# Kernel tuning notes

Measured on AMD Instinct MI355X. Metric: run time of the kernel, lower is better.

## Reference

```python
import jax, jax.numpy as jnp
import numpy as np

N_NODES = 25000
N_EDGES = 400000
D = 1024


def setup_inputs() -> dict:
    key = jax.random.key(0)
    ks = jax.random.split(key, 8)
    s = 1.0 / np.sqrt(D)
    return {
        "x": jax.random.normal(ks[0], (N_NODES, D), dtype=jnp.float32),
        "edge_src": jax.random.randint(ks[1], (N_EDGES,), 0, N_NODES, dtype=jnp.int32),
        "edge_dst": jax.random.randint(ks[2], (N_EDGES,), 0, N_NODES, dtype=jnp.int32),
        "W_self0": jax.random.normal(ks[3], (D, D), dtype=jnp.float32) * s,
        "W_neigh0": jax.random.normal(ks[4], (D, D), dtype=jnp.float32) * s,
        "b0": jnp.zeros((D,), dtype=jnp.float32),
        "W_self1": jax.random.normal(ks[5], (D, D), dtype=jnp.float32) * s,
        "W_neigh1": jax.random.normal(ks[6], (D, D), dtype=jnp.float32) * s,
        "b1": jnp.zeros((D,), dtype=jnp.float32),
    }


def _sage_layer(h, edge_src, edge_dst, deg_inv, W_self, W_neigh, b):
    # mean aggregation over in-neighbors: gather src feats, segment-sum by dst
    msg = h[edge_src]                                            # [E, d]
    agg = jax.ops.segment_sum(msg, edge_dst, num_segments=h.shape[0])  # [N, d]
    mean = agg * deg_inv[:, None]
    return h @ W_self + mean @ W_neigh + b


def reference(x, edge_src, edge_dst, W_self0, W_neigh0, b0, W_self1, W_neigh1, b1):
    N = x.shape[0]
    deg = jax.ops.segment_sum(jnp.ones_like(edge_dst, dtype=x.dtype), edge_dst, num_segments=N)
    deg_inv = 1.0 / jnp.maximum(deg, 1.0)  # isolated nodes -> 0 neighbor mean
    h = jax.nn.relu(_sage_layer(x, edge_src, edge_dst, deg_inv, W_self0, W_neigh0, b0))
    out = _sage_layer(h, edge_src, edge_dst, deg_inv, W_self1, W_neigh1, b1)
    return out
```

## Files before the change

kernel.cpp:

```cpp
#include <hip/hip_runtime.h>
#include <stdint.h>

#define NN 25000
#define NE 400000
#define DD 1024

typedef __attribute__((ext_vector_type(8))) short short8;
typedef __attribute__((ext_vector_type(4))) float f32x4;

__device__ __forceinline__ unsigned short f2bf(float f) {
  union { float f; uint32_t u; } v; v.f = f;
  uint32_t r = v.u + 0x7fffu + ((v.u >> 16) & 1u);
  return (unsigned short)(r >> 16);
}
__device__ __forceinline__ float bf2f(unsigned short h) {
  union { uint32_t u; float f; } v; v.u = ((uint32_t)h) << 16;
  return v.f;
}

__device__ __forceinline__ void gld_lds16(const void* g, void* l) {
  __builtin_amdgcn_global_load_lds(
      (const __attribute__((address_space(1))) void*)g,
      (__attribute__((address_space(3))) void*)l, 16, 0, 0);
}

__global__ __launch_bounds__(256) void k_cast_bf16(const float* __restrict__ in,
                                                   unsigned short* __restrict__ out,
                                                   int n8) {
  int i = blockIdx.x * blockDim.x + threadIdx.x;
  int stride = gridDim.x * blockDim.x;
  for (; i < n8; i += stride) {
    const float4* p = (const float4*)(in + (size_t)i * 8);
    float4 a = p[0], b = p[1];
    ushort4 r0, r1;
    r0.x = f2bf(a.x); r0.y = f2bf(a.y); r0.z = f2bf(a.z); r0.w = f2bf(a.w);
    r1.x = f2bf(b.x); r1.y = f2bf(b.y); r1.z = f2bf(b.z); r1.w = f2bf(b.w);
    ushort4* q = (ushort4*)(out + (size_t)i * 8);
    q[0] = r0; q[1] = r1;
  }
}

__global__ __launch_bounds__(256) void k_transcast(const float* __restrict__ W,
                                                   unsigned short* __restrict__ WT,
                                                   int kofs) {
  __shared__ unsigned short tile[64][66];
  int t = threadIdx.x;
  int k0 = blockIdx.x * 64, n0 = blockIdx.y * 64;
#pragma unroll
  for (int p = 0; p < 16; ++p) {
    int idx = p * 256 + t;
    int lr = idx >> 6, lc = idx & 63;
    tile[lr][lc] = f2bf(W[(size_t)(k0 + lr) * 1024 + n0 + lc]);
  }
  __syncthreads();
#pragma unroll
  for (int p = 0; p < 16; ++p) {
    int idx = p * 256 + t;
    int lr = idx >> 6, lc = idx & 63;
    WT[(size_t)(n0 + lr) * 2048 + kofs + k0 + lc] = tile[lc][lr];
  }
}

__global__ __launch_bounds__(256) void k_deg(const int* __restrict__ dst,
                                             int* __restrict__ deg, int E) {
  int i = blockIdx.x * blockDim.x + threadIdx.x;
  if (i < E) atomicAdd(&deg[dst[i]], 1);
}

__global__ __launch_bounds__(1024) void k_scan(const int* __restrict__ deg,
                                               int* __restrict__ rowptr,
                                               int* __restrict__ cursor,
                                               float* __restrict__ deg_inv, int N) {
  __shared__ int wsum[16];
  __shared__ int carry_s;
  int t = threadIdx.x, lane = t & 63, w = t >> 6;
  if (t == 0) carry_s = 0;
  __syncthreads();
  for (int base = 0; base < N; base += 1024) {
    int i = base + t;
    int v = (i < N) ? deg[i] : 0;
    int x = v;
#pragma unroll
    for (int off = 1; off < 64; off <<= 1) {
      int y = __shfl_up(x, off);
      if (lane >= off) x += y;
    }
    __syncthreads();
    if (lane == 63) wsum[w] = x;
    __syncthreads();
    if (w == 0 && lane < 16) {
      int s = wsum[lane];
#pragma unroll
      for (int off = 1; off < 16; off <<= 1) {
        int y = __shfl_up(s, off);
        if (lane >= off) s += y;
      }
      wsum[lane] = s;
    }
    __syncthreads();
    int wbase = (w > 0) ? wsum[w - 1] : 0;
    int incl = wbase + x;
    int carry = carry_s;
    if (i < N) {
      int excl = carry + incl - v;
      rowptr[i] = excl;
      cursor[i] = excl;
      deg_inv[i] = 1.0f / fmaxf((float)v, 1.0f);
    }
    __syncthreads();
    if (t == 1023) carry_s = carry + incl;
  }
  __syncthreads();
  if (t == 0) rowptr[N] = carry_s;
}

__global__ __launch_bounds__(256) void k_fill(const int* __restrict__ src,
                                              const int* __restrict__ dst,
                                              int* __restrict__ cursor,
                                              int* __restrict__ srcs, int E) {
  int i = blockIdx.x * blockDim.x + threadIdx.x;
  if (i < E) {
    int p = atomicAdd(&cursor[dst[i]], 1);
    srcs[p] = src[i];
  }
}

__global__ __launch_bounds__(256) void k_agg(const unsigned short* __restrict__ h,
                                             const int* __restrict__ rowptr,
                                             const int* __restrict__ srcs,
                                             const float* __restrict__ deg_inv,
                                             unsigned short* __restrict__ mean) {
  int node = blockIdx.x;
  int t = threadIdx.x;
  int beg = rowptr[node], end = rowptr[node + 1];
  int c = t * 4;
  float a0 = 0.f, a1 = 0.f, a2 = 0.f, a3 = 0.f;
  int e = beg;
  for (; e + 1 < end; e += 2) {
    int s0 = srcs[e], s1 = srcs[e + 1];
    ushort4 v0 = *(const ushort4*)(h + (size_t)s0 * DD + c);
    ushort4 v1 = *(const ushort4*)(h + (size_t)s1 * DD + c);
    a0 += bf2f(v0.x) + bf2f(v1.x);
    a1 += bf2f(v0.y) + bf2f(v1.y);
    a2 += bf2f(v0.z) + bf2f(v1.z);
    a3 += bf2f(v0.w) + bf2f(v1.w);
  }
  if (e < end) {
    int s0 = srcs[e];
    ushort4 v0 = *(const ushort4*)(h + (size_t)s0 * DD + c);
    a0 += bf2f(v0.x); a1 += bf2f(v0.y); a2 += bf2f(v0.z); a3 += bf2f(v0.w);
  }
  float di = deg_inv[node];
  ushort4 r;
  r.x = f2bf(a0 * di); r.y = f2bf(a1 * di); r.z = f2bf(a2 * di); r.w = f2bf(a3 * di);
  *(ushort4*)(mean + (size_t)node * DD + c) = r;
}

template <bool RELU, bool OUT_BF16>
__global__ __launch_bounds__(256) void k_gemm(const unsigned short* __restrict__ A1,
                                              const unsigned short* __restrict__ A2,
                                              const unsigned short* __restrict__ WT,
                                              const float* __restrict__ bias,
                                              void* __restrict__ Cout, int M) {
  __shared__ __align__(16) unsigned short lA[128 * 32];
  __shared__ __align__(16) unsigned short lB[128 * 32];
  const int t = threadIdx.x;
  const int lane = t & 63, wave = t >> 6;
  const int wm = wave >> 1, wn = wave & 1;
  const int bn = blockIdx.x, bm = blockIdx.y;
  const int fr = lane & 15, fq = lane >> 4;

  f32x4 acc[4][4];
#pragma unroll
  for (int m = 0; m < 4; ++m)
#pragma unroll
    for (int n = 0; n < 4; ++n) acc[m][n] = (f32x4){0.f, 0.f, 0.f, 0.f};

  const int srow = t >> 2;
  const int skk = (t & 3) * 8;
  int ar0 = bm * 128 + srow;
  int ar1 = ar0 + 64;
  if (ar0 > M - 1) ar0 = M - 1;
  if (ar1 > M - 1) ar1 = M - 1;
  const int br0 = bn * 128 + srow;
  const int br1 = br0 + 64;
  unsigned short* ldsA0 = lA + wave * 512;
  unsigned short* ldsA1 = lA + 2048 + wave * 512;
  unsigned short* ldsB0 = lB + wave * 512;
  unsigned short* ldsB1 = lB + 2048 + wave * 512;

  for (int kt = 0; kt < 64; ++kt) {
    const unsigned short* As = (kt < 32) ? A1 : A2;
    const int ka = (kt & 31) * 32 + skk;
    const int kw = kt * 32 + skk;
    __syncthreads();
    gld_lds16(As + (size_t)ar0 * 1024 + ka, ldsA0);
    gld_lds16(As + (size_t)ar1 * 1024 + ka, ldsA1);
    gld_lds16(WT + (size_t)br0 * 2048 + kw, ldsB0);
    gld_lds16(WT + (size_t)br1 * 2048 + kw, ldsB1);
    __syncthreads();

    short8 af[4], bfr[4];
#pragma unroll
    for (int m = 0; m < 4; ++m)
      af[m] = *(const short8*)&lA[(wm * 64 + m * 16 + fr) * 32 + fq * 8];
#pragma unroll
    for (int n = 0; n < 4; ++n)
      bfr[n] = *(const short8*)&lB[(wn * 64 + n * 16 + fr) * 32 + fq * 8];
#pragma unroll
    for (int m = 0; m < 4; ++m)
#pragma unroll
      for (int n = 0; n < 4; ++n)
        acc[m][n] = __builtin_amdgcn_mfma_f32_16x16x32_bf16(af[m], bfr[n], acc[m][n], 0, 0, 0);
  }

#pragma unroll
  for (int m = 0; m < 4; ++m) {
    int r0 = bm * 128 + wm * 64 + m * 16 + fq * 4;
#pragma unroll
    for (int j = 0; j < 4; ++j) {
      int r = r0 + j;
      if (r >= M) continue;
#pragma unroll
      for (int n = 0; n < 4; ++n) {
        int cc = bn * 128 + wn * 64 + n * 16 + fr;
        float v = acc[m][n][j] + bias[cc];
        if (RELU) v = fmaxf(v, 0.f);
        if (OUT_BF16)
          ((unsigned short*)Cout)[(size_t)r * 1024 + cc] = f2bf(v);
        else
          ((float*)Cout)[(size_t)r * 1024 + cc] = v;
      }
    }
  }
}

extern "C" void kernel_launch(void* const* d_in, const int* in_sizes, int n_in,
                              void* d_out, int out_size, void* d_ws, size_t ws_size,
                              hipStream_t stream) {
  const float* x = (const float*)d_in[0];
  const int* esrc = (const int*)d_in[1];
  const int* edst = (const int*)d_in[2];
  const float* Ws0 = (const float*)d_in[3];
  const float* Wn0 = (const float*)d_in[4];
  const float* b0 = (const float*)d_in[5];
  const float* Ws1 = (const float*)d_in[6];
  const float* Wn1 = (const float*)d_in[7];
  const float* b1 = (const float*)d_in[8];
  float* out = (float*)d_out;

  char* ws = (char*)d_ws;
  size_t off = 0;
  auto alloc = [&](size_t bytes) -> void* {
    void* p = ws + off;
    off = (off + bytes + 255) & ~(size_t)255;
    return p;
  };
  unsigned short* x_bf = (unsigned short*)alloc((size_t)NN * DD * 2);
  unsigned short* h_bf = (unsigned short*)alloc((size_t)NN * DD * 2);
  unsigned short* mean_bf = (unsigned short*)alloc((size_t)NN * DD * 2);
  unsigned short* WT0 = (unsigned short*)alloc((size_t)DD * 2048 * 2);
  unsigned short* WT1 = (unsigned short*)alloc((size_t)DD * 2048 * 2);
  int* deg = (int*)alloc((size_t)NN * 4);
  int* rowptr = (int*)alloc((size_t)(NN + 1) * 4);
  int* cursor = (int*)alloc((size_t)NN * 4);
  float* dinv = (float*)alloc((size_t)NN * 4);
  int* srcs = (int*)alloc((size_t)NE * 4);

  hipMemsetAsync(deg, 0, (size_t)NN * 4, stream);

  k_cast_bf16<<<2048, 256, 0, stream>>>(x, x_bf, NN * DD / 8);
  dim3 tg(16, 16);
  k_transcast<<<tg, 256, 0, stream>>>(Ws0, WT0, 0);
  k_transcast<<<tg, 256, 0, stream>>>(Wn0, WT0, 1024);
  k_transcast<<<tg, 256, 0, stream>>>(Ws1, WT1, 0);
  k_transcast<<<tg, 256, 0, stream>>>(Wn1, WT1, 1024);

  k_deg<<<(NE + 255) / 256, 256, 0, stream>>>(edst, deg, NE);
  k_scan<<<1, 1024, 0, stream>>>(deg, rowptr, cursor, dinv, NN);
  k_fill<<<(NE + 255) / 256, 256, 0, stream>>>(esrc, edst, cursor, srcs, NE);

  dim3 gg(8, (NN + 127) / 128);

  k_agg<<<NN, 256, 0, stream>>>(x_bf, rowptr, srcs, dinv, mean_bf);
  k_gemm<true, true><<<gg, 256, 0, stream>>>(x_bf, mean_bf, WT0, b0, (void*)h_bf, NN);

  k_agg<<<NN, 256, 0, stream>>>(h_bf, rowptr, srcs, dinv, mean_bf);
  k_gemm<false, false><<<gg, 256, 0, stream>>>(h_bf, mean_bf, WT1, b1, (void*)out, NN);
}
```

Before: 808.1 us.

## Parallelize degree scan, widen aggregation loads, double-buffer and remap GEMM tiles

The single-block prefix scan is replaced by a three-kernel multi-block scan. Aggregation now handles two nodes per block with 16-byte loads per thread. The GEMM double-buffers its LDS tiles so the next k-slice loads while MFMAs run, and it remaps the flat block index so consecutive blocks spread across column tiles (XCD-aware ordering). The cost is more LDS per block and extra kernel launches for the scan.

After: 786.7 us. -2.6%, faster.

```diff
diff --git a/kernel.cpp b/kernel.cpp
--- a/kernel.cpp
+++ b/kernel.cpp
@@ -67,51 +67,60 @@
   if (i < E) atomicAdd(&deg[dst[i]], 1);
 }
 
-__global__ __launch_bounds__(1024) void k_scan(const int* __restrict__ deg,
+__global__ __launch_bounds__(256) void k_scan1(const int* __restrict__ deg,
+                                               int* __restrict__ rowptr,
+                                               int* __restrict__ bsum, int N) {
+  __shared__ int ws[4];
+  int t = threadIdx.x, lane = t & 63, w = t >> 6;
+  int i = blockIdx.x * 256 + t;
+  int v = (i < N) ? deg[i] : 0;
+  int x = v;
+#pragma unroll
+  for (int off = 1; off < 64; off <<= 1) {
+    int y = __shfl_up(x, off);
+    if (lane >= off) x += y;
+  }
+  if (lane == 63) ws[w] = x;
+  __syncthreads();
+  int wbase = 0;
+#pragma unroll
+  for (int j = 0; j < 3; ++j)
+    if (w > j) wbase += ws[j];
+  if (i < N) rowptr[i] = wbase + x - v;
+  if (t == 255) bsum[blockIdx.x] = wbase + x;
+}
+
+__global__ __launch_bounds__(128) void k_scan2(const int* __restrict__ bsum,
+                                               int* __restrict__ boff,
+                                               int* __restrict__ rowptr_end, int nb) {
+  __shared__ int ws[2];
+  int t = threadIdx.x, lane = t & 63, w = t >> 6;
+  int v = (t < nb) ? bsum[t] : 0;
+  int x = v;
+#pragma unroll
+  for (int off = 1; off < 64; off <<= 1) {
+    int y = __shfl_up(x, off);
+    if (lane >= off) x += y;
+  }
+  if (lane == 63) ws[w] = x;
+  __syncthreads();
+  int wbase = (w == 1) ? ws[0] : 0;
+  if (t < nb) boff[t] = wbase + x - v;
+  if (t == 127) *rowptr_end = wbase + x;
+}
+
+__global__ __launch_bounds__(256) void k_scan3(const int* __restrict__ deg,
+                                               const int* __restrict__ boff,
                                                int* __restrict__ rowptr,
                                                int* __restrict__ cursor,
-                                               float* __restrict__ deg_inv, int N) {
-  __shared__ int wsum[16];
-  __shared__ int carry_s;
-  int t = threadIdx.x, lane = t & 63, w = t >> 6;
-  if (t == 0) carry_s = 0;
-  __syncthreads();
-  for (int base = 0; base < N; base += 1024) {
-    int i = base + t;
-    int v = (i < N) ? deg[i] : 0;
-    int x = v;
-#pragma unroll
-    for (int off = 1; off < 64; off <<= 1) {
-      int y = __shfl_up(x, off);
-      if (lane >= off) x += y;
-    }
-    __syncthreads();
-    if (lane == 63) wsum[w] = x;
-    __syncthreads();
-    if (w == 0 && lane < 16) {
-      int s = wsum[lane];
-#pragma unroll
-      for (int off = 1; off < 16; off <<= 1) {
-        int y = __shfl_up(s, off);
-        if (lane >= off) s += y;
-      }
-      wsum[lane] = s;
-    }
-    __syncthreads();
-    int wbase = (w > 0) ? wsum[w - 1] : 0;
-    int incl = wbase + x;
-    int carry = carry_s;
-    if (i < N) {
-      int excl = carry + incl - v;
-      rowptr[i] = excl;
-      cursor[i] = excl;
-      deg_inv[i] = 1.0f / fmaxf((float)v, 1.0f);
-    }
-    __syncthreads();
-    if (t == 1023) carry_s = carry + incl;
-  }
-  __syncthreads();
-  if (t == 0) rowptr[N] = carry_s;
+                                               float* __restrict__ dinv, int N) {
+  int i = blockIdx.x * 256 + threadIdx.x;
+  if (i < N) {
+    int r = rowptr[i] + boff[blockIdx.x];
+    rowptr[i] = r;
+    cursor[i] = r;
+    dinv[i] = 1.0f / fmaxf((float)deg[i], 1.0f);
+  }
 }
 
 __global__ __launch_bounds__(256) void k_fill(const int* __restrict__ src,
@@ -129,31 +138,35 @@
                                              const int* __restrict__ rowptr,
                                              const int* __restrict__ srcs,
                                              const float* __restrict__ deg_inv,
-                                             unsigned short* __restrict__ mean) {
-  int node = blockIdx.x;
-  int t = threadIdx.x;
+                                             unsigned short* __restrict__ mean, int N) {
+  int node = blockIdx.x * 2 + (threadIdx.x >> 7);
+  if (node >= N) return;
+  int t = threadIdx.x & 127;
+  int c = t * 8;
   int beg = rowptr[node], end = rowptr[node + 1];
-  int c = t * 4;
-  float a0 = 0.f, a1 = 0.f, a2 = 0.f, a3 = 0.f;
+  float a[8];
+#pragma unroll
+  for (int j = 0; j < 8; ++j) a[j] = 0.f;
   int e = beg;
   for (; e + 1 < end; e += 2) {
     int s0 = srcs[e], s1 = srcs[e + 1];
-    ushort4 v0 = *(const ushort4*)(h + (size_t)s0 * DD + c);
-    ushort4 v1 = *(const ushort4*)(h + (size_t)s1 * DD + c);
-    a0 += bf2f(v0.x) + bf2f(v1.x);
-    a1 += bf2f(v0.y) + bf2f(v1.y);
-    a2 += bf2f(v0.z) + bf2f(v1.z);
-    a3 += bf2f(v0.w) + bf2f(v1.w);
+    short8 v0 = *(const short8*)(h + (size_t)s0 * DD + c);
+    short8 v1 = *(const short8*)(h + (size_t)s1 * DD + c);
+#pragma unroll
+    for (int j = 0; j < 8; ++j)
+      a[j] += bf2f((unsigned short)v0[j]) + bf2f((unsigned short)v1[j]);
   }
   if (e < end) {
     int s0 = srcs[e];
-    ushort4 v0 = *(const ushort4*)(h + (size_t)s0 * DD + c);
-    a0 += bf2f(v0.x); a1 += bf2f(v0.y); a2 += bf2f(v0.z); a3 += bf2f(v0.w);
+    short8 v0 = *(const short8*)(h + (size_t)s0 * DD + c);
+#pragma unroll
+    for (int j = 0; j < 8; ++j) a[j] += bf2f((unsigned short)v0[j]);
   }
   float di = deg_inv[node];
-  ushort4 r;
-  r.x = f2bf(a0 * di); r.y = f2bf(a1 * di); r.z = f2bf(a2 * di); r.w = f2bf(a3 * di);
-  *(ushort4*)(mean + (size_t)node * DD + c) = r;
+  short8 r;
+#pragma unroll
+  for (int j = 0; j < 8; ++j) r[j] = (short)f2bf(a[j] * di);
+  *(short8*)(mean + (size_t)node * DD + c) = r;
 }
 
 template <bool RELU, bool OUT_BF16>
@@ -162,13 +175,17 @@
                                               const unsigned short* __restrict__ WT,
                                               const float* __restrict__ bias,
                                               void* __restrict__ Cout, int M) {
-  __shared__ __align__(16) unsigned short lA[128 * 32];
-  __shared__ __align__(16) unsigned short lB[128 * 32];
+  __shared__ __align__(16) unsigned short lA[2][128 * 32];
+  __shared__ __align__(16) unsigned short lB[2][128 * 32];
   const int t = threadIdx.x;
   const int lane = t & 63, wave = t >> 6;
   const int wm = wave >> 1, wn = wave & 1;
-  const int bn = blockIdx.x, bm = blockIdx.y;
   const int fr = lane & 15, fq = lane >> 4;
+
+  const int nbm = gridDim.x >> 3;
+  const int hw = blockIdx.x;
+  const int g = (hw & 7) * nbm + (hw >> 3);
+  const int bm = g >> 3, bn = g & 7;
 
   f32x4 acc[4][4];
 #pragma unroll
@@ -184,34 +201,39 @@
   if (ar1 > M - 1) ar1 = M - 1;
   const int br0 = bn * 128 + srow;
   const int br1 = br0 + 64;
-  unsigned short* ldsA0 = lA + wave * 512;
-  unsigned short* ldsA1 = lA + 2048 + wave * 512;
-  unsigned short* ldsB0 = lB + wave * 512;
-  unsigned short* ldsB1 = lB + 2048 + wave * 512;
-
-  for (int kt = 0; kt < 64; ++kt) {
+
+  auto stage = [&](int kt, int buf) {
     const unsigned short* As = (kt < 32) ? A1 : A2;
     const int ka = (kt & 31) * 32 + skk;
     const int kw = kt * 32 + skk;
+    unsigned short* dA = &lA[buf][wave * 512];
+    unsigned short* dB = &lB[buf][wave * 512];
+    gld_lds16(As + (size_t)ar0 * 1024 + ka, dA);
+    gld_lds16(As + (size_t)ar1 * 1024 + ka, dA + 2048);
+    gld_lds16(WT + (size_t)br0 * 2048 + kw, dB);
+    gld_lds16(WT + (size_t)br1 * 2048 + kw, dB + 2048);
+  };
+
+  stage(0, 0);
+  __syncthreads();
+  int cur = 0;
+#pragma unroll 2
+  for (int kt = 0; kt < 64; ++kt) {
+    if (kt < 63) stage(kt + 1, cur ^ 1);
+    short8 af[4], bfv[4];
+#pragma unroll
+    for (int m = 0; m < 4; ++m)
+      af[m] = *(const short8*)&lA[cur][(wm * 64 + m * 16 + fr) * 32 + fq * 8];
+#pragma unroll
+    for (int n = 0; n < 4; ++n)
+      bfv[n] = *(const short8*)&lB[cur][(wn * 64 + n * 16 + fr) * 32 + fq * 8];
+#pragma unroll
+    for (int m = 0; m < 4; ++m)
+#pragma unroll
+      for (int n = 0; n < 4; ++n)
+        acc[m][n] = __builtin_amdgcn_mfma_f32_16x16x32_bf16(af[m], bfv[n], acc[m][n], 0, 0, 0);
     __syncthreads();
-    gld_lds16(As + (size_t)ar0 * 1024 + ka, ldsA0);
-    gld_lds16(As + (size_t)ar1 * 1024 + ka, ldsA1);
-    gld_lds16(WT + (size_t)br0 * 2048 + kw, ldsB0);
-    gld_lds16(WT + (size_t)br1 * 2048 + kw, ldsB1);
-    __syncthreads();
-
-    short8 af[4], bfr[4];
-#pragma unroll
-    for (int m = 0; m < 4; ++m)
-      af[m] = *(const short8*)&lA[(wm * 64 + m * 16 + fr) * 32 + fq * 8];
-#pragma unroll
-    for (int n = 0; n < 4; ++n)
-      bfr[n] = *(const short8*)&lB[(wn * 64 + n * 16 + fr) * 32 + fq * 8];
-#pragma unroll
-    for (int m = 0; m < 4; ++m)
-#pragma unroll
-      for (int n = 0; n < 4; ++n)
-        acc[m][n] = __builtin_amdgcn_mfma_f32_16x16x32_bf16(af[m], bfr[n], acc[m][n], 0, 0, 0);
+    cur ^= 1;
   }
 
 #pragma unroll
@@ -266,6 +288,8 @@
   int* cursor = (int*)alloc((size_t)NN * 4);
   float* dinv = (float*)alloc((size_t)NN * 4);
   int* srcs = (int*)alloc((size_t)NE * 4);
+  int* bsum = (int*)alloc(128 * 4);
+  int* boff = (int*)alloc(128 * 4);
 
   hipMemsetAsync(deg, 0, (size_t)NN * 4, stream);
 
@@ -276,15 +300,19 @@
   k_transcast<<<tg, 256, 0, stream>>>(Ws1, WT1, 0);
   k_transcast<<<tg, 256, 0, stream>>>(Wn1, WT1, 1024);
 
+  const int nsb = (NN + 255) / 256;
   k_deg<<<(NE + 255) / 256, 256, 0, stream>>>(edst, deg, NE);
-  k_scan<<<1, 1024, 0, stream>>>(deg, rowptr, cursor, dinv, NN);
+  k_scan1<<<nsb, 256, 0, stream>>>(deg, rowptr, bsum, NN);
+  k_scan2<<<1, 128, 0, stream>>>(bsum, boff, rowptr + NN, nsb);
+  k_scan3<<<nsb, 256, 0, stream>>>(deg, boff, rowptr, cursor, dinv, NN);
   k_fill<<<(NE + 255) / 256, 256, 0, stream>>>(esrc, edst, cursor, srcs, NE);
 
-  dim3 gg(8, (NN + 127) / 128);
-
-  k_agg<<<NN, 256, 0, stream>>>(x_bf, rowptr, srcs, dinv, mean_bf);
+  const int nbm = (NN + 127) / 128;
+  dim3 gg(8 * nbm);
+
+  k_agg<<<(NN + 1) / 2, 256, 0, stream>>>(x_bf, rowptr, srcs, dinv, mean_bf, NN);
   k_gemm<true, true><<<gg, 256, 0, stream>>>(x_bf, mean_bf, WT0, b0, (void*)h_bf, NN);
 
-  k_agg<<<NN, 256, 0, stream>>>(h_bf, rowptr, srcs, dinv, mean_bf);
+  k_agg<<<(NN + 1) / 2, 256, 0, stream>>>(h_bf, rowptr, srcs, dinv, mean_bf, NN);
   k_gemm<false, false><<<gg, 256, 0, stream>>>(h_bf, mean_bf, WT1, b1, (void*)out, NN);
 }
```
